# Kernel tuning notes

Measured on AMD Instinct MI355X. Metric: run time of the kernel, lower is better.

## Reference

```python
import jax, jax.numpy as jnp
import numpy as np

DIM = 768
NUM_HEADS = 12
HEAD_DIM = DIM // NUM_HEADS
SCALE = HEAD_DIM ** -0.5


def setup_inputs() -> dict:
    key = jax.random.key(0)
    ks = jax.random.split(key, 7)
    B, N, C = 8, 1024, DIM
    x = jax.random.normal(ks[0], (B, N, C), dtype=jnp.float32)
    mask = jax.random.randint(ks[1], (B, N), 0, 2) > 0  # True = masked out
    qkv_w = jax.random.normal(ks[2], (3 * C, C), dtype=jnp.float32) * 0.02
    q_bias = jax.random.normal(ks[3], (C,), dtype=jnp.float32) * 0.02
    v_bias = jax.random.normal(ks[4], (C,), dtype=jnp.float32) * 0.02
    proj_w = jax.random.normal(ks[5], (C, C), dtype=jnp.float32) * 0.02
    proj_b = jax.random.normal(ks[6], (C,), dtype=jnp.float32) * 0.02
    return {"x": x, "mask": mask, "qkv_w": qkv_w, "q_bias": q_bias,
            "v_bias": v_bias, "proj_w": proj_w, "proj_b": proj_b}


def reference(x, mask, qkv_w, q_bias, v_bias, proj_w, proj_b):
    B, N, C = x.shape
    # CAE bias: concat(q_bias, zeros, v_bias) for the fused qkv projection
    qkv_bias = jnp.concatenate([q_bias, jnp.zeros_like(v_bias), v_bias])
    qkv = x @ qkv_w.T + qkv_bias  # [B, N, 3C]
    qkv = qkv.reshape(B, N, 3, NUM_HEADS, HEAD_DIM)
    q, k, v = (qkv[:, :, i].transpose(0, 2, 1, 3) for i in range(3))  # [B,H,N,hd]
    attn = jnp.einsum('bhqd,bhkd->bhqk', q * SCALE, k)  # [B,H,N,N]
    attn = jnp.where(mask[:, None, None, :], -jnp.inf, attn)
    attn = jax.nn.softmax(attn, axis=-1)
    out = jnp.einsum('bhqk,bhkd->bhqd', attn, v)  # [B,H,N,hd]
    out = out.transpose(0, 2, 1, 3).reshape(B, N, C)
    return out @ proj_w.T + proj_b
```

## Files before the change

### kernel.cpp

```cpp
#include <hip/hip_runtime.h>
#include <cstddef>
#include <cstdint>


typedef __attribute__((ext_vector_type(4))) float f32x4;
typedef __attribute__((ext_vector_type(8))) __bf16 bf16x8;
typedef __attribute__((ext_vector_type(4))) unsigned int uint4v;
typedef __attribute__((ext_vector_type(2))) unsigned int uint2v;

#define QK_PRESCALE 0.18033688011112042f

__device__ __forceinline__ unsigned short f2bf(float f) {
  return (unsigned short)((__float_as_uint(f) + 0x8000u) >> 16);
}
__device__ __forceinline__ unsigned int pack2bf(float flo, float fhi) {
  unsigned ulo = __float_as_uint(flo) + 0x8000u;
  unsigned uhi = __float_as_uint(fhi) + 0x8000u;
  return __builtin_amdgcn_perm(uhi, ulo, 0x07060302);
}

__device__ __forceinline__ void gl_lds16(const unsigned short* g, unsigned short* l) {
  __builtin_amdgcn_global_load_lds(
      (const __attribute__((address_space(1))) unsigned int*)g,
      (__attribute__((address_space(3))) unsigned int*)l, 16, 0, 0);
}

__global__ __launch_bounds__(256)
void cvt3_kernel(const float* __restrict__ s0, unsigned short* __restrict__ d0,
                 const float* __restrict__ s1, unsigned short* __restrict__ d1,
                 const float* __restrict__ s2, unsigned short* __restrict__ d2) {
  int bid = blockIdx.x;
  const float* s; unsigned short* d; int i; int n4;
  if (bid < 6144)      { s = s0; d = d0; i = bid * 256 + threadIdx.x;            n4 = 1572864; }
  else if (bid < 7872) { s = s1; d = d1; i = (bid - 6144) * 256 + threadIdx.x;   n4 = 442368; }
  else                 { s = s2; d = d2; i = (bid - 7872) * 256 + threadIdx.x;   n4 = 147456; }
  if (i < n4) {
    float4 v = ((const float4*)s)[i];
    uint2v o;
    o.x = pack2bf(v.x, v.y);
    o.y = pack2bf(v.z, v.w);
    ((uint2v*)d)[i] = o;
  }
}

__device__ __forceinline__ int a0row(int o) { return (o < 10) ? o * 8 : 144 + (o - 10) * 8; }
__device__ __forceinline__ int a1row(int o) { return (o < 8) ? 80 + o * 8 : 224 + (o - 8) * 8; }

__global__ __launch_bounds__(512, 2)
void qkv_gemm(const unsigned short* __restrict__ xb, const unsigned short* __restrict__ wb,
              const float* __restrict__ qb, const float* __restrict__ vb,
              unsigned short* __restrict__ qo, unsigned short* __restrict__ ko,
              unsigned short* __restrict__ vto) {
  __shared__ __align__(16) unsigned short lds[69632];
  const int tid = threadIdx.x;
  const int lane = tid & 63, wid = tid >> 6;
  const int widu = __builtin_amdgcn_readfirstlane(wid);
  const int lm = lane & 15, lq = lane >> 4;
  const int xsw = lm & 7;
  const int wr = widu >> 2, wc = widu & 3;
  const int L = blockIdx.x;
  const int xcd = L & 7, s = L >> 3;
  const int tt = xcd * 4 + (s >> 3);
  const int ft = s & 7;
  const int m0 = tt * 256;
  const int n0 = ft * 288;
  const int srow = lane >> 3;
  const int scolsw = ((lane & 7) ^ srow) * 8;
  const unsigned short* paS = wb + (size_t)(n0 + srow) * 768 + scolsw;
  const unsigned short* pbS = xb + (size_t)(m0 + srow) * 768 + scolsw;

  const int a0n3 = (widu < 4);
  const int a0o = a0n3 ? widu * 3 : 12 + (widu - 4) * 2;
  const int a0r0 = a0row(a0o), a0r1 = a0row(a0o + 1);
  const int a0r2 = a0n3 ? a0row(a0o + 2) : 0;
  const int a1r0 = a1row(2 * widu), a1r1 = a1row(2 * widu + 1);
  const int b0q0 = (2 * widu) >> 2, b0q1 = (2 * widu + 1) >> 2;
  const int b0r0 = b0q0 * 64 + ((2 * widu) & 3) * 8;
  const int b0r1 = b0q1 * 64 + ((2 * widu + 1) & 3) * 8;
  const int b1r0 = b0r0 + 32, b1r1 = b0r1 + 32;

  f32x4 acc[9][4] = {};

#define STAGE_A0(tgt) { const size_t _c = (size_t)(tgt) * 64; const int _b = ((tgt) & 1) * 18432; \
    gl_lds16(paS + (size_t)a0r0 * 768 + _c, &lds[_b + a0r0 * 64]); \
    gl_lds16(paS + (size_t)a0r1 * 768 + _c, &lds[_b + a0r1 * 64]); \
    if (a0n3) gl_lds16(paS + (size_t)a0r2 * 768 + _c, &lds[_b + a0r2 * 64]); }

#define STAGE_A1(tgt) { const size_t _c = (size_t)(tgt) * 64; const int _b = ((tgt) & 1) * 18432; \
    gl_lds16(paS + (size_t)a1r0 * 768 + _c, &lds[_b + a1r0 * 64]); \
    gl_lds16(paS + (size_t)a1r1 * 768 + _c, &lds[_b + a1r1 * 64]); }

#define STAGE_B0(tgt) { const size_t _c = (size_t)(tgt) * 64; const int _b = 36864 + ((tgt) & 1) * 16384; \
    gl_lds16(pbS + (size_t)b0r0 * 768 + _c, &lds[_b + b0r0 * 64]); \
    gl_lds16(pbS + (size_t)b0r1 * 768 + _c, &lds[_b + b0r1 * 64]); }

#define STAGE_B1(tgt) { const size_t _c = (size_t)(tgt) * 64; const int _b = 36864 + ((tgt) & 1) * 16384; \
    gl_lds16(pbS + (size_t)b1r0 * 768 + _c, &lds[_b + b1r0 * 64]); \
    gl_lds16(pbS + (size_t)b1r1 * 768 + _c, &lds[_b + b1r1 * 64]); }

#define PHASE_COMPUTE(R0, NR, CB, bufb) { \
    const unsigned short* _Ab = &lds[(bufb) * 18432]; \
    const unsigned short* _Bb = &lds[36864 + (bufb) * 16384]; \
    bf16x8 af[NR][2], bff[2][2]; \
    _Pragma("unroll") for (int m2 = 0; m2 < (NR); ++m2) \
      _Pragma("unroll") for (int kx = 0; kx < 2; ++kx) \
        af[m2][kx] = *(const bf16x8*)&_Ab[(wr * 144 + ((R0) + m2) * 16 + lm) * 64 + (((kx * 4 + lq) ^ xsw) * 8)]; \
    _Pragma("unroll") for (int n2 = 0; n2 < 2; ++n2) \
      _Pragma("unroll") for (int kx = 0; kx < 2; ++kx) \
        bff[n2][kx] = *(const bf16x8*)&_Bb[(wc * 64 + ((CB) * 2 + n2) * 16 + lm) * 64 + (((kx * 4 + lq) ^ xsw) * 8)]; \
    __builtin_amdgcn_s_setprio(1); \
    _Pragma("unroll") for (int kx = 0; kx < 2; ++kx) \
      _Pragma("unroll") for (int m2 = 0; m2 < (NR); ++m2) \
        _Pragma("unroll") for (int n2 = 0; n2 < 2; ++n2) \
          acc[(R0) + m2][(CB) * 2 + n2] = __builtin_amdgcn_mfma_f32_16x16x32_bf16( \
              af[m2][kx], bff[n2][kx], acc[(R0) + m2][(CB) * 2 + n2], 0, 0, 0); \
    __builtin_amdgcn_s_setprio(0); }

#define WAIT_Q0() { if (a0n3) asm volatile("s_waitcnt vmcnt(7)" ::: "memory"); \
                    else      asm volatile("s_waitcnt vmcnt(6)" ::: "memory"); \
                    asm volatile("s_barrier" ::: "memory"); }
#define WAIT_Q1() { if (a0n3) asm volatile("s_waitcnt vmcnt(5)" ::: "memory"); \
                    else      asm volatile("s_waitcnt vmcnt(4)" ::: "memory"); \
                    asm volatile("s_barrier" ::: "memory"); }
#define BAR_A()   asm volatile("s_barrier" ::: "memory")
#define BAR_B()   asm volatile("s_waitcnt lgkmcnt(0)\ns_barrier" ::: "memory")

  STAGE_A0(0); STAGE_B0(0); STAGE_A1(0); STAGE_B1(0);

  for (int t = 0; t < 12; ++t) {
    const int b = t & 1;
    const int tn = (t < 11) ? t + 1 : 11;
    STAGE_A0(tn);
    WAIT_Q0();
    PHASE_COMPUTE(0, 5, 0, b);
    BAR_B();
    STAGE_B0(tn);
    WAIT_Q1();
    PHASE_COMPUTE(0, 5, 1, b);
    BAR_B();
    STAGE_A1(tn);
    BAR_A();
    PHASE_COMPUTE(5, 4, 0, b);
    BAR_B();
    STAGE_B1(tn);
    BAR_A();
    PHASE_COMPUTE(5, 4, 1, b);
    BAR_B();
  }
  asm volatile("s_waitcnt vmcnt(0)" ::: "memory");

#undef STAGE_A0
#undef STAGE_A1
#undef STAGE_B0
#undef STAGE_B1
#undef PHASE_COMPUTE

  const int bq = tt >> 2;
  const int tokb = (tt & 3) * 256;
#pragma unroll
  for (int mi = 0; mi < 9; ++mi) {
    const int fblk = n0 + wr * 144 + mi * 16;
    if (fblk < 1536) {
      const bool isq = fblk < 768;
      unsigned short* dst0 = isq ? qo : ko;
      const int fd = fblk - (isq ? 0 : 768);
      const int hh = fd >> 6;
      const int dih = (fd & 63) + lq * 4;
      f32x4 bias4 = {0.f, 0.f, 0.f, 0.f};
      if (isq) bias4 = *(const f32x4*)&qb[fblk + lq * 4];
#pragma unroll
      for (int ni = 0; ni < 4; ++ni) {
        const int tok = tokb + wc * 64 + ni * 16 + lm;
        uint2v pk;
        if (isq) {
          pk.x = pack2bf((acc[mi][ni][0] + bias4[0]) * QK_PRESCALE,
                         (acc[mi][ni][1] + bias4[1]) * QK_PRESCALE);
          pk.y = pack2bf((acc[mi][ni][2] + bias4[2]) * QK_PRESCALE,
                         (acc[mi][ni][3] + bias4[3]) * QK_PRESCALE);
        } else {
          pk.x = pack2bf(acc[mi][ni][0], acc[mi][ni][1]);
          pk.y = pack2bf(acc[mi][ni][2], acc[mi][ni][3]);
        }
        *(uint2v*)&dst0[(((size_t)(bq * 12 + hh)) * 1024 + tok) * 64 + dih] = pk;
      }
    }
  }
  if (n0 + 288 > 1536) {
#pragma unroll
    for (int p = 0; p < 2; ++p) {
      __syncthreads();
      if (wr == p) {
#pragma unroll
        for (int mi = 0; mi < 9; ++mi) {
          const int fblk = n0 + p * 144 + mi * 16;
          if (fblk >= 1536) {
            f32x4 bias4 = *(const f32x4*)&vb[fblk - 1536 + lq * 4];
#pragma unroll
            for (int ni = 0; ni < 4; ++ni) {
              const int tokl = wc * 64 + ni * 16 + lm;
#pragma unroll
              for (int r = 0; r < 4; ++r)
                lds[(mi * 16 + lq * 4 + r) * 264 + tokl] = f2bf(acc[mi][ni][r] + bias4[r]);
            }
          }
        }
      }
      __syncthreads();
      const int fv = 1536 - (n0 + p * 144);
      const int rv0 = fv > 0 ? fv : 0;
      for (int r = rv0 + (tid >> 2); r < 144; r += 128) {
        const int tq = tid & 3;
        const int dgv = n0 + p * 144 + r - 1536;
        const int hh = dgv >> 6, d = dgv & 63;
        unsigned short* dstv = vto + (((size_t)(bq * 12 + hh)) * 64 + d) * 1024 + tokb + tq * 64;
        const unsigned short* srcr = &lds[r * 264 + tq * 64];
#pragma unroll
        for (int j = 0; j < 8; ++j)
          *(uint4v*)&dstv[j * 8] = *(const uint4v*)&srcr[j * 8];
      }
    }
  }
}

__global__ __launch_bounds__(256)
void attn_mfma(const unsigned short* __restrict__ q, const unsigned short* __restrict__ k,
               const unsigned short* __restrict__ vt, const int* __restrict__ mask,
               unsigned short* __restrict__ ao) {
  __shared__ unsigned short ks_s[64 * 64];
  __shared__ unsigned short vs_s[64 * 64];
  __shared__ unsigned short ps[4][32 * 72];
  __shared__ float mkl[64];
  const int tid = threadIdx.x;
  const int lane = tid & 63, wid = tid >> 6;
  const int lm = lane & 15, lq = lane >> 4;
  const int xsw = lm & 7;
  const int L = blockIdx.x;
  const int xcd = L & 7, s = L >> 3;
  const int bh = xcd * 12 + s / 8;
  const int qt = s % 8;
  const int bb = bh / 12, hh = bh % 12;
  const unsigned short* qp = q + (size_t)bh * 65536;
  const unsigned short* kp = k + (size_t)bh * 65536;
  const unsigned short* vp = vt + (size_t)bh * 65536;
  const int* mp = mask + bb * 1024;
  const int q0 = qt * 128 + wid * 32;
  const int srow = lane >> 3;
  const int scolsw = ((lane & 7) ^ srow) * 8;
  const unsigned short* gk = kp + (size_t)(wid * 16 + srow) * 64 + scolsw;
  const unsigned short* gv = vp + (size_t)(wid * 16 + srow) * 1024 + scolsw;

  bf16x8 qf[2][2];
#pragma unroll
  for (int mi = 0; mi < 2; ++mi)
#pragma unroll
    for (int ks2 = 0; ks2 < 2; ++ks2)
      qf[mi][ks2] = *(const bf16x8*)&qp[(size_t)(q0 + mi * 16 + lm) * 64 + ks2 * 32 + lq * 8];
  bf16x8 ones;
#pragma unroll
  for (int i = 0; i < 8; ++i) ones[i] = (__bf16)1.0f;

  f32x4 o_acc[2][4] = {};
  f32x4 l_acc[2] = {};

  for (int kt = 0; kt < 16; ++kt) {
    __syncthreads();
#pragma unroll
    for (int i = 0; i < 2; ++i) {
      gl_lds16(gk + (size_t)kt * 4096 + (size_t)i * 8 * 64, &ks_s[(wid * 16 + i * 8) * 64]);
      gl_lds16(gv + (size_t)kt * 64 + (size_t)i * 8 * 1024, &vs_s[(wid * 16 + i * 8) * 64]);
    }
    if (tid < 64) mkl[tid] = mp[kt * 64 + tid] ? -1e30f : 0.0f;
    __syncthreads();

    f32x4 st[4][2] = {};
#pragma unroll
    for (int ks2 = 0; ks2 < 2; ++ks2) {
      bf16x8 kf[4];
#pragma unroll
      for (int nt = 0; nt < 4; ++nt)
        kf[nt] = *(const bf16x8*)&ks_s[(nt * 16 + lm) * 64 + (((ks2 * 4 + lq) ^ xsw) * 8)];
#pragma unroll
      for (int nt = 0; nt < 4; ++nt)
#pragma unroll
        for (int mi = 0; mi < 2; ++mi)
          st[nt][mi] = __builtin_amdgcn_mfma_f32_16x16x32_bf16(kf[nt], qf[mi][ks2], st[nt][mi], 0, 0, 0);
    }

#pragma unroll
    for (int nt = 0; nt < 4; ++nt) {
      f32x4 mv4 = *(const f32x4*)&mkl[nt * 16 + lq * 4];
#pragma unroll
      for (int mi = 0; mi < 2; ++mi) {
        uint2v pk;
        pk.x = pack2bf(__builtin_amdgcn_exp2f(st[nt][mi][0] + mv4[0]),
                       __builtin_amdgcn_exp2f(st[nt][mi][1] + mv4[1]));
        pk.y = pack2bf(__builtin_amdgcn_exp2f(st[nt][mi][2] + mv4[2]),
                       __builtin_amdgcn_exp2f(st[nt][mi][3] + mv4[3]));
        *(uint2v*)&ps[wid][(mi * 16 + lm) * 72 + nt * 16 + lq * 4] = pk;
      }
    }

#pragma unroll
    for (int ks2 = 0; ks2 < 2; ++ks2) {
      bf16x8 pf[2], vf[4];
#pragma unroll
      for (int mi = 0; mi < 2; ++mi)
        pf[mi] = *(const bf16x8*)&ps[wid][(mi * 16 + lm) * 72 + ks2 * 32 + lq * 8];
#pragma unroll
      for (int nt = 0; nt < 4; ++nt)
        vf[nt] = *(const bf16x8*)&vs_s[(nt * 16 + lm) * 64 + (((ks2 * 4 + lq) ^ xsw) * 8)];
#pragma unroll
      for (int mi = 0; mi < 2; ++mi) {
#pragma unroll
        for (int nt = 0; nt < 4; ++nt)
          o_acc[mi][nt] = __builtin_amdgcn_mfma_f32_16x16x32_bf16(pf[mi], vf[nt], o_acc[mi][nt], 0, 0, 0);
        l_acc[mi] = __builtin_amdgcn_mfma_f32_16x16x32_bf16(pf[mi], ones, l_acc[mi], 0, 0, 0);
      }
    }
  }

#pragma unroll
  for (int mi = 0; mi < 2; ++mi) {
#pragma unroll
    for (int r = 0; r < 4; ++r) {
      float inv = 1.0f / l_acc[mi][r];
      int tok = q0 + mi * 16 + lq * 4 + r;
#pragma unroll
      for (int nt = 0; nt < 4; ++nt)
        ao[(size_t)(bb * 1024 + tok) * 768 + hh * 64 + nt * 16 + lm] = f2bf(o_acc[mi][nt][r] * inv);
    }
  }
}

__global__ __launch_bounds__(256)
void proj_gemm(const unsigned short* __restrict__ ab, const unsigned short* __restrict__ wb,
               const float* __restrict__ pb, float* __restrict__ out) {
  __shared__ unsigned short as[128 * 64];
  __shared__ unsigned short bs[128 * 64];
  const int tid = threadIdx.x;
  const int lane = tid & 63, wid = tid >> 6;
  const int lm = lane & 15, lq = lane >> 4;
  const int xsw = lm & 7;
  const int wm = (wid & 1) * 64, wn = (wid >> 1) * 64;
  const int L = blockIdx.x;
  const int xcd = L & 7, s = L >> 3;
  const int m0 = (xcd * 8 + s / 6) * 128;
  const int n0 = (s % 6) * 128;
  const int srow = lane >> 3;
  const int scolsw = ((lane & 7) ^ srow) * 8;
  const unsigned short* ga = wb + (size_t)(n0 + wid * 32 + srow) * 768 + scolsw;
  const unsigned short* gb = ab + (size_t)(m0 + wid * 32 + srow) * 768 + scolsw;
  f32x4 acc[4][4] = {};
  for (int kt = 0; kt < 768; kt += 64) {
#pragma unroll
    for (int i = 0; i < 4; ++i) {
      gl_lds16(ga + kt + (size_t)i * 8 * 768, &as[(wid * 32 + i * 8) * 64]);
      gl_lds16(gb + kt + (size_t)i * 8 * 768, &bs[(wid * 32 + i * 8) * 64]);
    }
    __syncthreads();
#pragma unroll
    for (int ks = 0; ks < 2; ++ks) {
      bf16x8 af[4], bf[4];
#pragma unroll
      for (int i = 0; i < 4; ++i)
        af[i] = *(const bf16x8*)&as[(wm + i * 16 + lm) * 64 + (((ks * 4 + lq) ^ xsw) * 8)];
#pragma unroll
      for (int i = 0; i < 4; ++i)
        bf[i] = *(const bf16x8*)&bs[(wn + i * 16 + lm) * 64 + (((ks * 4 + lq) ^ xsw) * 8)];
#pragma unroll
      for (int mi = 0; mi < 4; ++mi)
#pragma unroll
        for (int ni = 0; ni < 4; ++ni)
          acc[mi][ni] = __builtin_amdgcn_mfma_f32_16x16x32_bf16(af[mi], bf[ni], acc[mi][ni], 0, 0, 0);
    }
    __syncthreads();
  }
#pragma unroll
  for (int mi = 0; mi < 4; ++mi) {
    int gn0 = n0 + wm + mi * 16 + lq * 4;
    f32x4 bias4 = *(const f32x4*)&pb[gn0];
#pragma unroll
    for (int ni = 0; ni < 4; ++ni) {
      int gm = m0 + wn + ni * 16 + lm;
      f32x4 o;
      o[0] = acc[mi][ni][0] + bias4[0];
      o[1] = acc[mi][ni][1] + bias4[1];
      o[2] = acc[mi][ni][2] + bias4[2];
      o[3] = acc[mi][ni][3] + bias4[3];
      *(f32x4*)&out[(size_t)gm * 768 + gn0] = o;
    }
  }
}

extern "C" void kernel_launch(void* const* d_in, const int* in_sizes, int n_in,
                              void* d_out, int out_size, void* d_ws, size_t ws_size,
                              hipStream_t stream) {
  const float* x      = (const float*)d_in[0];
  const int*   mask   = (const int*)d_in[1];
  const float* qkv_w  = (const float*)d_in[2];
  const float* q_bias = (const float*)d_in[3];
  const float* v_bias = (const float*)d_in[4];
  const float* proj_w = (const float*)d_in[5];
  const float* proj_b = (const float*)d_in[6];
  float* out = (float*)d_out;
  unsigned short* p = (unsigned short*)d_ws;
  unsigned short* xb     = p;              p += 6291456;
  unsigned short* wqkvb  = p;              p += 1769472;
  unsigned short* wprojb = p;              p += 589824;
  unsigned short* qo     = p;              p += 6291456;
  unsigned short* ko     = p;              p += 6291456;
  unsigned short* vto    = p;              p += 6291456;
  unsigned short* ao     = p;

  cvt3_kernel<<<8448, 256, 0, stream>>>(x, xb, qkv_w, wqkvb, proj_w, wprojb);
  qkv_gemm<<<256, 512, 0, stream>>>(xb, wqkvb, q_bias, v_bias, qo, ko, vto);
  attn_mfma<<<768, 256, 0, stream>>>(qo, ko, vto, mask, ao);
  proj_gemm<<<384, 256, 0, stream>>>(ao, wprojb, proj_b, out);
}
```

Baseline: 184.3 us.

## Restructure GEMM main loop to two-tile-ahead prefetch with fewer barriers

Replaces the four-phase-per-tile loop, which had a barrier after each quarter-compute, with one compute block per K-tile. All B fragments and A rows are read from LDS up front. The second half of the next tile is staged mid-iteration and the first half of the tile two steps ahead is staged after a single end-of-iteration barrier. This cuts barrier and wait overhead and deepens the global-to-LDS prefetch. In exchange it holds more fragments in registers, which can raise register pressure, and the clamped tail redundantly reloads the last tile.

```diff
diff --git a/kernel.cpp b/kernel.cpp
--- a/kernel.cpp
+++ b/kernel.cpp
@@ -98,54 +98,65 @@
     gl_lds16(pbS + (size_t)b1r0 * 768 + _c, &lds[_b + b1r0 * 64]); \
     gl_lds16(pbS + (size_t)b1r1 * 768 + _c, &lds[_b + b1r1 * 64]); }
 
-#define PHASE_COMPUTE(R0, NR, CB, bufb) { \
-    const unsigned short* _Ab = &lds[(bufb) * 18432]; \
-    const unsigned short* _Bb = &lds[36864 + (bufb) * 16384]; \
-    bf16x8 af[NR][2], bff[2][2]; \
-    _Pragma("unroll") for (int m2 = 0; m2 < (NR); ++m2) \
-      _Pragma("unroll") for (int kx = 0; kx < 2; ++kx) \
-        af[m2][kx] = *(const bf16x8*)&_Ab[(wr * 144 + ((R0) + m2) * 16 + lm) * 64 + (((kx * 4 + lq) ^ xsw) * 8)]; \
-    _Pragma("unroll") for (int n2 = 0; n2 < 2; ++n2) \
-      _Pragma("unroll") for (int kx = 0; kx < 2; ++kx) \
-        bff[n2][kx] = *(const bf16x8*)&_Bb[(wc * 64 + ((CB) * 2 + n2) * 16 + lm) * 64 + (((kx * 4 + lq) ^ xsw) * 8)]; \
-    __builtin_amdgcn_s_setprio(1); \
-    _Pragma("unroll") for (int kx = 0; kx < 2; ++kx) \
-      _Pragma("unroll") for (int m2 = 0; m2 < (NR); ++m2) \
-        _Pragma("unroll") for (int n2 = 0; n2 < 2; ++n2) \
-          acc[(R0) + m2][(CB) * 2 + n2] = __builtin_amdgcn_mfma_f32_16x16x32_bf16( \
-              af[m2][kx], bff[n2][kx], acc[(R0) + m2][(CB) * 2 + n2], 0, 0, 0); \
-    __builtin_amdgcn_s_setprio(0); }
-
-#define WAIT_Q0() { if (a0n3) asm volatile("s_waitcnt vmcnt(7)" ::: "memory"); \
-                    else      asm volatile("s_waitcnt vmcnt(6)" ::: "memory"); \
-                    asm volatile("s_barrier" ::: "memory"); }
-#define WAIT_Q1() { if (a0n3) asm volatile("s_waitcnt vmcnt(5)" ::: "memory"); \
-                    else      asm volatile("s_waitcnt vmcnt(4)" ::: "memory"); \
-                    asm volatile("s_barrier" ::: "memory"); }
-#define BAR_A()   asm volatile("s_barrier" ::: "memory")
-#define BAR_B()   asm volatile("s_waitcnt lgkmcnt(0)\ns_barrier" ::: "memory")
+#define WAIT_G() { if (a0n3) asm volatile("s_waitcnt vmcnt(5)" ::: "memory"); \
+                   else      asm volatile("s_waitcnt vmcnt(4)" ::: "memory"); \
+                   asm volatile("s_barrier" ::: "memory"); }
+#define BAR_E()   asm volatile("s_waitcnt lgkmcnt(0)\ns_barrier" ::: "memory")
 
   STAGE_A0(0); STAGE_B0(0); STAGE_A1(0); STAGE_B1(0);
+  STAGE_A0(1); STAGE_B0(1);
+  WAIT_G();
 
   for (int t = 0; t < 12; ++t) {
     const int b = t & 1;
-    const int tn = (t < 11) ? t + 1 : 11;
-    STAGE_A0(tn);
-    WAIT_Q0();
-    PHASE_COMPUTE(0, 5, 0, b);
-    BAR_B();
-    STAGE_B0(tn);
-    WAIT_Q1();
-    PHASE_COMPUTE(0, 5, 1, b);
-    BAR_B();
-    STAGE_A1(tn);
-    BAR_A();
-    PHASE_COMPUTE(5, 4, 0, b);
-    BAR_B();
-    STAGE_B1(tn);
-    BAR_A();
-    PHASE_COMPUTE(5, 4, 1, b);
-    BAR_B();
+    const int tn1 = (t + 1 < 12) ? t + 1 : 11;
+    const int tn2 = (t + 2 < 12) ? t + 2 : 11;
+    const unsigned short* Ab = &lds[b * 18432];
+    const unsigned short* Bb = &lds[36864 + b * 16384];
+
+    bf16x8 bff[4][2], af[5][2];
+#pragma unroll
+    for (int n2 = 0; n2 < 4; ++n2)
+#pragma unroll
+      for (int kx = 0; kx < 2; ++kx)
+        bff[n2][kx] = *(const bf16x8*)&Bb[(wc * 64 + n2 * 16 + lm) * 64 + (((kx * 4 + lq) ^ xsw) * 8)];
+#pragma unroll
+    for (int m2 = 0; m2 < 5; ++m2)
+#pragma unroll
+      for (int kx = 0; kx < 2; ++kx)
+        af[m2][kx] = *(const bf16x8*)&Ab[(wr * 144 + m2 * 16 + lm) * 64 + (((kx * 4 + lq) ^ xsw) * 8)];
+
+    STAGE_A1(tn1); STAGE_B1(tn1);
+
+    __builtin_amdgcn_s_setprio(1);
+#pragma unroll
+    for (int kx = 0; kx < 2; ++kx)
+#pragma unroll
+      for (int m2 = 0; m2 < 5; ++m2)
+#pragma unroll
+        for (int n2 = 0; n2 < 4; ++n2)
+          acc[m2][n2] = __builtin_amdgcn_mfma_f32_16x16x32_bf16(af[m2][kx], bff[n2][kx], acc[m2][n2], 0, 0, 0);
+    __builtin_amdgcn_s_setprio(0);
+
+    bf16x8 af2[4][2];
+#pragma unroll
+    for (int m2 = 0; m2 < 4; ++m2)
+#pragma unroll
+      for (int kx = 0; kx < 2; ++kx)
+        af2[m2][kx] = *(const bf16x8*)&Ab[(wr * 144 + (5 + m2) * 16 + lm) * 64 + (((kx * 4 + lq) ^ xsw) * 8)];
+    __builtin_amdgcn_s_setprio(1);
+#pragma unroll
+    for (int kx = 0; kx < 2; ++kx)
+#pragma unroll
+      for (int m2 = 0; m2 < 4; ++m2)
+#pragma unroll
+        for (int n2 = 0; n2 < 4; ++n2)
+          acc[5 + m2][n2] = __builtin_amdgcn_mfma_f32_16x16x32_bf16(af2[m2][kx], bff[n2][kx], acc[5 + m2][n2], 0, 0, 0);
+    __builtin_amdgcn_s_setprio(0);
+
+    BAR_E();
+    STAGE_A0(tn2); STAGE_B0(tn2);
+    WAIT_G();
   }
   asm volatile("s_waitcnt vmcnt(0)" ::: "memory");
 
@@ -153,7 +164,6 @@
 #undef STAGE_A1
 #undef STAGE_B0
 #undef STAGE_B1
-#undef PHASE_COMPUTE
 
   const int bq = tt >> 2;
   const int tokb = (tt & 3) * 256;
```

After: 183.1 us. About the same (-0.7%).
